# Optimization experiments

Hardware: AMD Instinct MI355X
Metric: run time of the kernel (lower is better)

## Reference

```python
import jax, jax.numpy as jnp
import numpy as np

N_NODES = 100000
HID = 128
N_EDGES = 600000


def sage_conv(h, src, dst, Wl, bl, Wr, n_nodes):
    # PyG SAGEConv (mean aggr): out = lin_l(mean_{j->i} h_j) + lin_r(h_i)
    msgs = h[src]                                               # [E, d] gather
    agg = jax.ops.segment_sum(msgs, dst, num_segments=n_nodes)  # [N, d]
    cnt = jax.ops.segment_sum(jnp.ones((src.shape[0], 1), h.dtype), dst,
                              num_segments=n_nodes)             # [N, 1]
    mean = agg / jnp.maximum(cnt, 1.0)                          # isolated nodes -> 0
    return mean @ Wl.T + bl + h @ Wr.T


def setup_inputs() -> dict:
    key = jax.random.key(0)
    ks = jax.random.split(key, 8)
    scale = 1.0 / np.sqrt(HID)
    x = jnp.arange(N_NODES, dtype=jnp.int64) if jax.config.jax_enable_x64 else jnp.arange(N_NODES, dtype=jnp.int32)
    edge_index = jax.random.randint(ks[0], (2, N_EDGES), 0, N_NODES)
    emb = jax.random.normal(ks[1], (N_NODES, HID), dtype=jnp.float32) * scale
    Wl1 = jax.random.normal(ks[2], (HID, HID), dtype=jnp.float32) * scale
    bl1 = jnp.zeros((HID,), jnp.float32)
    Wr1 = jax.random.normal(ks[3], (HID, HID), dtype=jnp.float32) * scale
    Wl2 = jax.random.normal(ks[4], (HID, HID), dtype=jnp.float32) * scale
    bl2 = jnp.zeros((HID,), jnp.float32)
    Wr2 = jax.random.normal(ks[5], (HID, HID), dtype=jnp.float32) * scale
    return {"x": x, "edge_index": edge_index, "emb": emb,
            "Wl1": Wl1, "bl1": bl1, "Wr1": Wr1,
            "Wl2": Wl2, "bl2": bl2, "Wr2": Wr2}


def reference(x, edge_index, emb, Wl1, bl1, Wr1, Wl2, bl2, Wr2):
    src, dst = edge_index[0], edge_index[1]
    n = emb.shape[0]
    h = emb[x]                                          # embedding lookup [N, d]
    h = jax.nn.relu(sage_conv(h, src, dst, Wl1, bl1, Wr1, n))  # dropout = eval identity
    h = jax.nn.relu(sage_conv(h, src, dst, Wl2, bl2, Wr2, n))
    return h
```

## Files before the change

### kernel.cpp

```cpp
#include <hip/hip_runtime.h>

#define HID 128

typedef unsigned short ushort_t;
typedef unsigned int uint_t;
typedef float f32x4 __attribute__((ext_vector_type(4)));
typedef short s16x8 __attribute__((ext_vector_type(8)));

__device__ __forceinline__ ushort_t f2bf(float f) {
  uint_t u = __float_as_uint(f);
  uint_t r = (u + 0x7FFFu + ((u >> 16) & 1u)) >> 16;
  return (ushort_t)r;
}
__device__ __forceinline__ float bfLo(uint_t v) { return __uint_as_float(v << 16); }
__device__ __forceinline__ float bfHi(uint_t v) { return __uint_as_float(v & 0xFFFF0000u); }

__global__ __launch_bounds__(256) void prep_kernel(
    const float* __restrict__ emb, const int* __restrict__ x,
    ushort_t* __restrict__ hb, int N,
    const float* __restrict__ Wl1, const float* __restrict__ Wr1,
    const float* __restrict__ Wl2, const float* __restrict__ Wr2,
    ushort_t* __restrict__ wsw,
    const int* __restrict__ dst, int* __restrict__ deg, int E) {
  int tid = blockIdx.x * 256 + threadIdx.x;
  const int halfN = (N + 1) >> 1;
  int gthreads = halfN * 16;
  if (tid < gthreads) {
    int r0 = tid >> 4, j = (tid & 15) * 8;
    int r1 = r0 + halfN;
    int s0 = x[r0];
    int s1 = (r1 < N) ? x[r1] : s0;
    const float* src0 = &emb[(size_t)s0 * HID + j];
    const float* src1 = &emb[(size_t)s1 * HID + j];
    float4 a0 = *(const float4*)src0;
    float4 a1 = *(const float4*)(src0 + 4);
    float4 b0 = *(const float4*)src1;
    float4 b1 = *(const float4*)(src1 + 4);
    uint4 p;
    p.x = (uint_t)f2bf(a0.x) | ((uint_t)f2bf(a0.y) << 16);
    p.y = (uint_t)f2bf(a0.z) | ((uint_t)f2bf(a0.w) << 16);
    p.z = (uint_t)f2bf(a1.x) | ((uint_t)f2bf(a1.y) << 16);
    p.w = (uint_t)f2bf(a1.z) | ((uint_t)f2bf(a1.w) << 16);
    *(uint4*)&hb[(size_t)r0 * HID + j] = p;
    if (r1 < N) {
      uint4 q;
      q.x = (uint_t)f2bf(b0.x) | ((uint_t)f2bf(b0.y) << 16);
      q.y = (uint_t)f2bf(b0.z) | ((uint_t)f2bf(b0.w) << 16);
      q.z = (uint_t)f2bf(b1.x) | ((uint_t)f2bf(b1.y) << 16);
      q.w = (uint_t)f2bf(b1.z) | ((uint_t)f2bf(b1.w) << 16);
      *(uint4*)&hb[(size_t)r1 * HID + j] = q;
    }
    return;
  }
  tid -= gthreads;
  if (tid < 65536) {
    const float* srcs[4] = {Wl1, Wr1, Wl2, Wr2};
    int m = tid >> 14, idx = tid & 16383;
    int j = idx & 7;
    int lane = (idx >> 3) & 63;
    int nt = (idx >> 9) & 7;
    int ks = (idx >> 12) & 3;
    int row = nt * 16 + (lane & 15);
    int col = ks * 32 + (lane >> 4) * 8 + j;
    wsw[tid] = f2bf(srcs[m][row * HID + col]);
    return;
  }
  tid -= 65536;
  if (tid < E) atomicAdd(&deg[dst[tid]], 1);
}

__global__ __launch_bounds__(256) void scan1_kernel(
    const int* __restrict__ deg, int* __restrict__ offsets,
    int* __restrict__ sums, int N) {
  __shared__ int s[256];
  int b = blockIdx.x, t = threadIdx.x;
  int base = b * 1024 + t * 4;
  int v0 = 0, v1 = 0, v2 = 0, v3 = 0;
  if (base + 0 < N) v0 = deg[base + 0];
  if (base + 1 < N) v1 = deg[base + 1];
  if (base + 2 < N) v2 = deg[base + 2];
  if (base + 3 < N) v3 = deg[base + 3];
  int mySum = v0 + v1 + v2 + v3;
  s[t] = mySum;
  __syncthreads();
  for (int off = 1; off < 256; off <<= 1) {
    int v = (t >= off) ? s[t - off] : 0;
    __syncthreads();
    s[t] += v;
    __syncthreads();
  }
  int excl = s[t] - mySum;
  if (t == 255) sums[b] = s[255];
  if (base + 0 < N) offsets[base + 0] = excl;
  if (base + 1 < N) offsets[base + 1] = excl + v0;
  if (base + 2 < N) offsets[base + 2] = excl + v0 + v1;
  if (base + 3 < N) offsets[base + 3] = excl + v0 + v1 + v2;
}

__global__ __launch_bounds__(256) void scan3_kernel(
    int* __restrict__ offsets, const int* __restrict__ sums,
    int* __restrict__ cursor, int N, int E, int nb) {
  __shared__ int red[256];
  int t = threadIdx.x;
  int chunk = (blockIdx.x * 256) >> 10;
  red[t] = (t < chunk) ? sums[t] : 0;
  __syncthreads();
  for (int off = 128; off > 0; off >>= 1) {
    if (t < off) red[t] += red[t + off];
    __syncthreads();
  }
  int prefix = red[0];
  int i = blockIdx.x * 256 + t;
  if (i < N) {
    int v = offsets[i] + prefix;
    offsets[i] = v;
    cursor[i] = v;
  } else if (i == N) {
    offsets[N] = E;
  }
}

__global__ __launch_bounds__(256) void fill_kernel(
    const int* __restrict__ src, const int* __restrict__ dst,
    int* __restrict__ cursor, int* __restrict__ csr, int E) {
  int e = blockIdx.x * 256 + threadIdx.x;
  if (e >= E) return;
  int d = dst[e];
  int pos = atomicAdd(&cursor[d], 1);
  csr[pos] = src[e];
}

__global__ __launch_bounds__(256) void aggregate_kernel(
    const ushort_t* __restrict__ hb, const int* __restrict__ offsets,
    const int* __restrict__ csr, ushort_t* __restrict__ meanb, int N) {
  int t = threadIdx.x;
  int node = blockIdx.x * 16 + (t >> 4);
  if (node >= N) return;
  int l15 = t & 15;
  int o0 = offsets[node], o1 = offsets[node + 1];

  float acc[8];
#pragma unroll
  for (int i = 0; i < 8; i++) acc[i] = 0.f;

  int e = o0;
  for (; e + 3 < o1; e += 4) {
    int s0 = csr[e], s1 = csr[e + 1], s2 = csr[e + 2], s3 = csr[e + 3];
    uint4 v0 = *(const uint4*)&hb[(size_t)s0 * HID + l15 * 8];
    uint4 v1 = *(const uint4*)&hb[(size_t)s1 * HID + l15 * 8];
    uint4 v2 = *(const uint4*)&hb[(size_t)s2 * HID + l15 * 8];
    uint4 v3 = *(const uint4*)&hb[(size_t)s3 * HID + l15 * 8];
    acc[0] += (bfLo(v0.x) + bfLo(v1.x)) + (bfLo(v2.x) + bfLo(v3.x));
    acc[1] += (bfHi(v0.x) + bfHi(v1.x)) + (bfHi(v2.x) + bfHi(v3.x));
    acc[2] += (bfLo(v0.y) + bfLo(v1.y)) + (bfLo(v2.y) + bfLo(v3.y));
    acc[3] += (bfHi(v0.y) + bfHi(v1.y)) + (bfHi(v2.y) + bfHi(v3.y));
    acc[4] += (bfLo(v0.z) + bfLo(v1.z)) + (bfLo(v2.z) + bfLo(v3.z));
    acc[5] += (bfHi(v0.z) + bfHi(v1.z)) + (bfHi(v2.z) + bfHi(v3.z));
    acc[6] += (bfLo(v0.w) + bfLo(v1.w)) + (bfLo(v2.w) + bfLo(v3.w));
    acc[7] += (bfHi(v0.w) + bfHi(v1.w)) + (bfHi(v2.w) + bfHi(v3.w));
  }
  if (e + 1 < o1) {
    int s0 = csr[e], s1 = csr[e + 1];
    uint4 v0 = *(const uint4*)&hb[(size_t)s0 * HID + l15 * 8];
    uint4 v1 = *(const uint4*)&hb[(size_t)s1 * HID + l15 * 8];
    acc[0] += bfLo(v0.x) + bfLo(v1.x);
    acc[1] += bfHi(v0.x) + bfHi(v1.x);
    acc[2] += bfLo(v0.y) + bfLo(v1.y);
    acc[3] += bfHi(v0.y) + bfHi(v1.y);
    acc[4] += bfLo(v0.z) + bfLo(v1.z);
    acc[5] += bfHi(v0.z) + bfHi(v1.z);
    acc[6] += bfLo(v0.w) + bfLo(v1.w);
    acc[7] += bfHi(v0.w) + bfHi(v1.w);
    e += 2;
  }
  if (e < o1) {
    int s0 = csr[e];
    uint4 v0 = *(const uint4*)&hb[(size_t)s0 * HID + l15 * 8];
    acc[0] += bfLo(v0.x); acc[1] += bfHi(v0.x);
    acc[2] += bfLo(v0.y); acc[3] += bfHi(v0.y);
    acc[4] += bfLo(v0.z); acc[5] += bfHi(v0.z);
    acc[6] += bfLo(v0.w); acc[7] += bfHi(v0.w);
  }

  int d = o1 - o0;
  float inv = 1.0f / (float)(d > 1 ? d : 1);
  uint4 p;
  p.x = (uint_t)f2bf(acc[0] * inv) | ((uint_t)f2bf(acc[1] * inv) << 16);
  p.y = (uint_t)f2bf(acc[2] * inv) | ((uint_t)f2bf(acc[3] * inv) << 16);
  p.z = (uint_t)f2bf(acc[4] * inv) | ((uint_t)f2bf(acc[5] * inv) << 16);
  p.w = (uint_t)f2bf(acc[6] * inv) | ((uint_t)f2bf(acc[7] * inv) << 16);
  *(uint4*)&meanb[(size_t)node * HID + l15 * 8] = p;
}

__global__ __launch_bounds__(256) void mfma_gemm_kernel(
    const ushort_t* __restrict__ meanb, const ushort_t* __restrict__ hb,
    const ushort_t* __restrict__ WlS, const ushort_t* __restrict__ WrS,
    const float* __restrict__ bias, float* __restrict__ outF,
    ushort_t* __restrict__ outB, int N, int outIsBf16) {
  __shared__ ushort_t ws[32768];
  const int t = threadIdx.x;
  const int wave = t >> 6;
  const int lane = t & 63;
  const int rowBase = (blockIdx.x * 4 + wave) * 32;
  const int l15 = lane & 15;
  const int quad = lane >> 4;
  const int kq = quad * 8;
  const bool active = rowBase < N;

  int r0 = rowBase + l15;       if (r0 >= N) r0 = N - 1;
  int r1 = rowBase + 16 + l15;  if (r1 >= N) r1 = N - 1;

  s16x8 a[2][2][4];
  if (active) {
#pragma unroll
    for (int ks = 0; ks < 4; ks++) {
      a[0][0][ks] = *(const s16x8*)&meanb[(size_t)r0 * HID + ks * 32 + kq];
      a[0][1][ks] = *(const s16x8*)&meanb[(size_t)r1 * HID + ks * 32 + kq];
      a[1][0][ks] = *(const s16x8*)&hb[(size_t)r0 * HID + ks * 32 + kq];
      a[1][1][ks] = *(const s16x8*)&hb[(size_t)r1 * HID + ks * 32 + kq];
    }
  }

#pragma unroll
  for (int it = 0; it < 8; it++) {
    int o = (it * 256 + t) * 8;
    *(s16x8*)&ws[o] = *(const s16x8*)&WlS[o];
    *(s16x8*)&ws[16384 + o] = *(const s16x8*)&WrS[o];
  }
  __syncthreads();

  if (active) {
    f32x4 acc[2][8];
#pragma unroll
    for (int mt = 0; mt < 2; mt++)
#pragma unroll
      for (int nt = 0; nt < 8; nt++) acc[mt][nt] = (f32x4){0.f, 0.f, 0.f, 0.f};

#pragma unroll
    for (int half = 0; half < 2; half++) {
      const int hbase = half * 16384;
#pragma unroll
      for (int ks = 0; ks < 4; ks++)
#pragma unroll
        for (int nt = 0; nt < 8; nt++) {
          s16x8 b = *(const s16x8*)&ws[hbase + ((ks * 8 + nt) * 64 + lane) * 8];
          acc[0][nt] = __builtin_amdgcn_mfma_f32_16x16x32_bf16(a[half][0][ks], b, acc[0][nt], 0, 0, 0);
          acc[1][nt] = __builtin_amdgcn_mfma_f32_16x16x32_bf16(a[half][1][ks], b, acc[1][nt], 0, 0, 0);
        }
    }

#pragma unroll
    for (int mt = 0; mt < 2; mt++) {
#pragma unroll
      for (int nt = 0; nt < 8; nt++) {
        int col = nt * 16 + l15;
        float bv = bias[col];
#pragma unroll
        for (int r = 0; r < 4; r++) {
          int row = rowBase + mt * 16 + quad * 4 + r;
          if (row < N) {
            float v = fmaxf(acc[mt][nt][r] + bv, 0.f);
            if (outIsBf16) outB[(size_t)row * HID + col] = f2bf(v);
            else           outF[(size_t)row * HID + col] = v;
          }
        }
      }
    }
  }
}

extern "C" void kernel_launch(void* const* d_in, const int* in_sizes, int n_in,
                              void* d_out, int out_size, void* d_ws, size_t ws_size,
                              hipStream_t stream) {
  const int* x = (const int*)d_in[0];
  const int* ei = (const int*)d_in[1];
  const float* emb = (const float*)d_in[2];
  const float* Wl1 = (const float*)d_in[3];
  const float* bl1 = (const float*)d_in[4];
  const float* Wr1 = (const float*)d_in[5];
  const float* Wl2 = (const float*)d_in[6];
  const float* bl2 = (const float*)d_in[7];
  const float* Wr2 = (const float*)d_in[8];
  float* out = (float*)d_out;

  const int N = in_sizes[0];
  const int E = in_sizes[1] / 2;
  const int* srcI = ei;
  const int* dstI = ei + E;

  char* p = (char*)d_ws;
  ushort_t* hb = (ushort_t*)p;    p += (size_t)N * HID * sizeof(ushort_t);
  ushort_t* meanb = (ushort_t*)p; p += (size_t)N * HID * sizeof(ushort_t);
  ushort_t* wb = (ushort_t*)p;    p += (size_t)4 * 16384 * sizeof(ushort_t);
  int* deg = (int*)p;             p += (size_t)((N + 3) & ~3) * sizeof(int);
  int* offsets = (int*)p;         p += (size_t)((N + 4) & ~3) * sizeof(int);
  int* cursor = (int*)p;          p += (size_t)((N + 3) & ~3) * sizeof(int);
  int* csr = (int*)p;             p += (size_t)((E + 3) & ~3) * sizeof(int);
  int* sums = (int*)p;            p += 256 * sizeof(int);

  ushort_t* Wlb1 = wb;
  ushort_t* Wrb1 = wb + 16384;
  ushort_t* Wlb2 = wb + 32768;
  ushort_t* Wrb2 = wb + 49152;

  const int nScanBlocks = (N + 1023) / 1024;
  const int eBlocks = (E + 255) / 256;
  const int gemmBlocks = (N + 127) / 128;
  const int aggBlocks = (N + 15) / 16;
  const int halfN = (N + 1) / 2;
  const int prepBlocks = (halfN * 16 + 65536 + E + 255) / 256;

  hipMemsetAsync(deg, 0, (size_t)N * sizeof(int), stream);
  prep_kernel<<<prepBlocks, 256, 0, stream>>>(emb, x, hb, N,
                                              Wl1, Wr1, Wl2, Wr2, wb,
                                              dstI, deg, E);
  scan1_kernel<<<nScanBlocks, 256, 0, stream>>>(deg, offsets, sums, N);
  scan3_kernel<<<(N + 256) / 256, 256, 0, stream>>>(offsets, sums, cursor,
                                                    N, E, nScanBlocks);
  fill_kernel<<<eBlocks, 256, 0, stream>>>(srcI, dstI, cursor, csr, E);

  aggregate_kernel<<<aggBlocks, 256, 0, stream>>>(hb, offsets, csr, meanb, N);
  mfma_gemm_kernel<<<gemmBlocks, 256, 0, stream>>>(meanb, hb, Wlb1, Wrb1, bl1,
                                                   nullptr, hb, N, 1);

  aggregate_kernel<<<aggBlocks, 256, 0, stream>>>(hb, offsets, csr, meanb, N);
  mfma_gemm_kernel<<<gemmBlocks, 256, 0, stream>>>(meanb, hb, Wlb2, Wrb2, bl2,
                                                   out, nullptr, N, 0);
}
```

Measured before the change: 293.6 us.

## Halve GEMM LDS footprint, widen prep gather per thread, double-buffer hidden state

The GEMM kernel now stages only one 32 KB weight matrix in LDS at a time, loading Wl, computing, syncing, then loading Wr. This halves shared memory per block to allow more resident blocks. The prep kernel gathers four embedding rows per thread instead of two to raise memory-level parallelism. Layer-1 output goes to a separate buffer rather than overwriting hb in place, which removes a read-write race across blocks but adds an extra N×128 bf16 workspace and an extra barrier in the GEMM.

```diff
diff --git a/kernel.cpp b/kernel.cpp
--- a/kernel.cpp
+++ b/kernel.cpp
@@ -14,6 +14,15 @@
 }
 __device__ __forceinline__ float bfLo(uint_t v) { return __uint_as_float(v << 16); }
 __device__ __forceinline__ float bfHi(uint_t v) { return __uint_as_float(v & 0xFFFF0000u); }
+
+__device__ __forceinline__ uint4 pack8(const float4& lo, const float4& hi) {
+  uint4 p;
+  p.x = (uint_t)f2bf(lo.x) | ((uint_t)f2bf(lo.y) << 16);
+  p.y = (uint_t)f2bf(lo.z) | ((uint_t)f2bf(lo.w) << 16);
+  p.z = (uint_t)f2bf(hi.x) | ((uint_t)f2bf(hi.y) << 16);
+  p.w = (uint_t)f2bf(hi.z) | ((uint_t)f2bf(hi.w) << 16);
+  return p;
+}
 
 __global__ __launch_bounds__(256) void prep_kernel(
     const float* __restrict__ emb, const int* __restrict__ x,
@@ -23,33 +32,27 @@
     ushort_t* __restrict__ wsw,
     const int* __restrict__ dst, int* __restrict__ deg, int E) {
   int tid = blockIdx.x * 256 + threadIdx.x;
-  const int halfN = (N + 1) >> 1;
-  int gthreads = halfN * 16;
+  const int qN = (N + 3) >> 2;
+  int gthreads = qN * 16;
   if (tid < gthreads) {
     int r0 = tid >> 4, j = (tid & 15) * 8;
-    int r1 = r0 + halfN;
+    int r1 = r0 + qN, r2 = r0 + 2 * qN, r3 = r0 + 3 * qN;
     int s0 = x[r0];
     int s1 = (r1 < N) ? x[r1] : s0;
-    const float* src0 = &emb[(size_t)s0 * HID + j];
-    const float* src1 = &emb[(size_t)s1 * HID + j];
-    float4 a0 = *(const float4*)src0;
-    float4 a1 = *(const float4*)(src0 + 4);
-    float4 b0 = *(const float4*)src1;
-    float4 b1 = *(const float4*)(src1 + 4);
-    uint4 p;
-    p.x = (uint_t)f2bf(a0.x) | ((uint_t)f2bf(a0.y) << 16);
-    p.y = (uint_t)f2bf(a0.z) | ((uint_t)f2bf(a0.w) << 16);
-    p.z = (uint_t)f2bf(a1.x) | ((uint_t)f2bf(a1.y) << 16);
-    p.w = (uint_t)f2bf(a1.z) | ((uint_t)f2bf(a1.w) << 16);
-    *(uint4*)&hb[(size_t)r0 * HID + j] = p;
-    if (r1 < N) {
-      uint4 q;
-      q.x = (uint_t)f2bf(b0.x) | ((uint_t)f2bf(b0.y) << 16);
-      q.y = (uint_t)f2bf(b0.z) | ((uint_t)f2bf(b0.w) << 16);
-      q.z = (uint_t)f2bf(b1.x) | ((uint_t)f2bf(b1.y) << 16);
-      q.w = (uint_t)f2bf(b1.z) | ((uint_t)f2bf(b1.w) << 16);
-      *(uint4*)&hb[(size_t)r1 * HID + j] = q;
-    }
+    int s2 = (r2 < N) ? x[r2] : s0;
+    int s3 = (r3 < N) ? x[r3] : s0;
+    const float* p0 = &emb[(size_t)s0 * HID + j];
+    const float* p1 = &emb[(size_t)s1 * HID + j];
+    const float* p2 = &emb[(size_t)s2 * HID + j];
+    const float* p3 = &emb[(size_t)s3 * HID + j];
+    float4 a0 = *(const float4*)p0, a1 = *(const float4*)(p0 + 4);
+    float4 b0 = *(const float4*)p1, b1 = *(const float4*)(p1 + 4);
+    float4 c0 = *(const float4*)p2, c1 = *(const float4*)(p2 + 4);
+    float4 d0 = *(const float4*)p3, d1 = *(const float4*)(p3 + 4);
+    *(uint4*)&hb[(size_t)r0 * HID + j] = pack8(a0, a1);
+    if (r1 < N) *(uint4*)&hb[(size_t)r1 * HID + j] = pack8(b0, b1);
+    if (r2 < N) *(uint4*)&hb[(size_t)r2 * HID + j] = pack8(c0, c1);
+    if (r3 < N) *(uint4*)&hb[(size_t)r3 * HID + j] = pack8(d0, d1);
     return;
   }
   tid -= gthreads;
@@ -197,7 +200,7 @@
     const ushort_t* __restrict__ WlS, const ushort_t* __restrict__ WrS,
     const float* __restrict__ bias, float* __restrict__ outF,
     ushort_t* __restrict__ outB, int N, int outIsBf16) {
-  __shared__ ushort_t ws[32768];
+  __shared__ ushort_t ws[16384];
   const int t = threadIdx.x;
   const int wave = t >> 6;
   const int lane = t & 63;
@@ -221,34 +224,35 @@
     }
   }
 
-#pragma unroll
-  for (int it = 0; it < 8; it++) {
-    int o = (it * 256 + t) * 8;
-    *(s16x8*)&ws[o] = *(const s16x8*)&WlS[o];
-    *(s16x8*)&ws[16384 + o] = *(const s16x8*)&WrS[o];
-  }
-  __syncthreads();
-
-  if (active) {
-    f32x4 acc[2][8];
-#pragma unroll
-    for (int mt = 0; mt < 2; mt++)
-#pragma unroll
-      for (int nt = 0; nt < 8; nt++) acc[mt][nt] = (f32x4){0.f, 0.f, 0.f, 0.f};
-
-#pragma unroll
-    for (int half = 0; half < 2; half++) {
-      const int hbase = half * 16384;
+  f32x4 acc[2][8];
+#pragma unroll
+  for (int mt = 0; mt < 2; mt++)
+#pragma unroll
+    for (int nt = 0; nt < 8; nt++) acc[mt][nt] = (f32x4){0.f, 0.f, 0.f, 0.f};
+
+#pragma unroll
+  for (int half = 0; half < 2; half++) {
+    const ushort_t* W = half ? WrS : WlS;
+#pragma unroll
+    for (int it = 0; it < 8; it++) {
+      int o = (it * 256 + t) * 8;
+      *(s16x8*)&ws[o] = *(const s16x8*)&W[o];
+    }
+    __syncthreads();
+    if (active) {
 #pragma unroll
       for (int ks = 0; ks < 4; ks++)
 #pragma unroll
         for (int nt = 0; nt < 8; nt++) {
-          s16x8 b = *(const s16x8*)&ws[hbase + ((ks * 8 + nt) * 64 + lane) * 8];
+          s16x8 b = *(const s16x8*)&ws[((ks * 8 + nt) * 64 + lane) * 8];
           acc[0][nt] = __builtin_amdgcn_mfma_f32_16x16x32_bf16(a[half][0][ks], b, acc[0][nt], 0, 0, 0);
           acc[1][nt] = __builtin_amdgcn_mfma_f32_16x16x32_bf16(a[half][1][ks], b, acc[1][nt], 0, 0, 0);
         }
     }
-
+    if (half == 0) __syncthreads();
+  }
+
+  if (active) {
 #pragma unroll
     for (int mt = 0; mt < 2; mt++) {
 #pragma unroll
@@ -290,6 +294,7 @@
 
   char* p = (char*)d_ws;
   ushort_t* hb = (ushort_t*)p;    p += (size_t)N * HID * sizeof(ushort_t);
+  ushort_t* hb2 = (ushort_t*)p;   p += (size_t)N * HID * sizeof(ushort_t);
   ushort_t* meanb = (ushort_t*)p; p += (size_t)N * HID * sizeof(ushort_t);
   ushort_t* wb = (ushort_t*)p;    p += (size_t)4 * 16384 * sizeof(ushort_t);
   int* deg = (int*)p;             p += (size_t)((N + 3) & ~3) * sizeof(int);
@@ -307,8 +312,8 @@
   const int eBlocks = (E + 255) / 256;
   const int gemmBlocks = (N + 127) / 128;
   const int aggBlocks = (N + 15) / 16;
-  const int halfN = (N + 1) / 2;
-  const int prepBlocks = (halfN * 16 + 65536 + E + 255) / 256;
+  const int qN = (N + 3) / 4;
+  const int prepBlocks = (qN * 16 + 65536 + E + 255) / 256;
 
   hipMemsetAsync(deg, 0, (size_t)N * sizeof(int), stream);
   prep_kernel<<<prepBlocks, 256, 0, stream>>>(emb, x, hb, N,
@@ -321,9 +326,9 @@
 
   aggregate_kernel<<<aggBlocks, 256, 0, stream>>>(hb, offsets, csr, meanb, N);
   mfma_gemm_kernel<<<gemmBlocks, 256, 0, stream>>>(meanb, hb, Wlb1, Wrb1, bl1,
-                                                   nullptr, hb, N, 1);
-
-  aggregate_kernel<<<aggBlocks, 256, 0, stream>>>(hb, offsets, csr, meanb, N);
-  mfma_gemm_kernel<<<gemmBlocks, 256, 0, stream>>>(meanb, hb, Wlb2, Wrb2, bl2,
+                                                   nullptr, hb2, N, 1);
+
+  aggregate_kernel<<<aggBlocks, 256, 0, stream>>>(hb2, offsets, csr, meanb, N);
+  mfma_gemm_kernel<<<gemmBlocks, 256, 0, stream>>>(meanb, hb2, Wlb2, Wrb2, bl2,
                                                    out, nullptr, N, 0);
 }
```

New measurement: 295.4 us. Within noise of the previous version (+0.6%).
